# Kernel tuning notes

Hardware: AMD Instinct MI355X
Metric: run time of the kernel (lower is better)

The kernel has to match this reference:

```python
import jax, jax.numpy as jnp
import numpy as np

LOG2 = np.float32(np.log(2.0))

def _jsd_pos(p):
    # get_positive_expectation, measure='JSD', average=False
    return LOG2 - jax.nn.softplus(-p)

def setup_inputs() -> dict:
    key = jax.random.key(0)
    k1, k2, k3, k4, k5, k6 = jax.random.split(key, 6)
    N, G, D = 65536, 512, 256
    batch_1 = jnp.sort(jax.random.randint(k1, (N,), 0, G))
    batch_2 = jnp.sort(jax.random.randint(k2, (N,), 0, G))
    z1 = jax.random.normal(k3, (N, D), dtype=jnp.float32)
    z2 = jax.random.normal(k4, (N, D), dtype=jnp.float32)
    g1 = jax.random.normal(k5, (G, D), dtype=jnp.float32)
    g2 = jax.random.normal(k6, (G, D), dtype=jnp.float32)
    return {"batch_1": batch_1, "batch_2": batch_2, "z1": z1, "z2": z2, "g1": g1, "g2": g2}

def reference(batch_1, batch_2, z1, z2, g1, g2):
    # pos_mask scatter-build -> dense one-hot [N, G]
    pos_mask_1 = jax.nn.one_hot(batch_1, g1.shape[0], dtype=z1.dtype)
    pos_mask_2 = jax.nn.one_hot(batch_2, g2.shape[0], dtype=z2.dtype)
    # masked node-graph similarity matrices [N, G]
    self_sim_1 = (z1 @ g1.T) * pos_mask_1
    self_sim_2 = (z2 @ g2.T) * pos_mask_2
    cross_sim_12 = (z1 @ g2.T) * pos_mask_1
    cross_sim_21 = (z2 @ g1.T) * pos_mask_2
    # sep=True branch: per-node row sums, L2 distance over nodes
    self_js_11 = _jsd_pos(self_sim_1).sum(1)
    cross_js_12 = _jsd_pos(cross_sim_12).sum(1)
    self_js_22 = _jsd_pos(self_sim_2).sum(1)
    cross_js_21 = _jsd_pos(cross_sim_21).sum(1)
    L_1 = jnp.sqrt(jnp.sum((self_js_11 - cross_js_12) ** 2))
    L_2 = jnp.sqrt(jnp.sum((self_js_22 - cross_js_21) ** 2))
    return L_1 + L_2
```

## Files before the change

kernel.cpp:

```cpp
#include <hip/hip_runtime.h>
#include <math.h>

__device__ __forceinline__ float jsd_pos(float p) {
    float sp = fmaxf(-p, 0.0f) + log1pf(expf(-fabsf(p)));
    return 0.69314718055994531f - sp;
}

#define NBLOCKS 2048
#define NODES_PER_WAVE 8

__global__ __launch_bounds__(256) void jsd_dot_kernel(
    const int*   __restrict__ b1,
    const int*   __restrict__ b2,
    const float* __restrict__ z1,
    const float* __restrict__ z2,
    const float* __restrict__ g1,
    const float* __restrict__ g2,
    float*       __restrict__ partials)
{
    const int wave = threadIdx.x >> 6;
    const int lane = threadIdx.x & 63;
    const int w    = blockIdx.x * 4 + wave;

    float acc1 = 0.0f, acc2 = 0.0f;

    #pragma unroll
    for (int j = 0; j < NODES_PER_WAVE; ++j) {
        const int node = w * NODES_PER_WAVE + j;

        const int i1 = b1[node];
        const int i2 = b2[node];

        const float4 a1  = ((const float4*)(z1 + (size_t)node * 256))[lane];
        const float4 a2  = ((const float4*)(z2 + (size_t)node * 256))[lane];
        const float4 w11 = ((const float4*)(g1 + (size_t)i1 * 256))[lane];
        const float4 w12 = ((const float4*)(g2 + (size_t)i1 * 256))[lane];
        const float4 w22 = ((const float4*)(g2 + (size_t)i2 * 256))[lane];
        const float4 w21 = ((const float4*)(g1 + (size_t)i2 * 256))[lane];

        float s11 = a1.x*w11.x + a1.y*w11.y + a1.z*w11.z + a1.w*w11.w;
        float c12 = a1.x*w12.x + a1.y*w12.y + a1.z*w12.z + a1.w*w12.w;
        float s22 = a2.x*w22.x + a2.y*w22.y + a2.z*w22.z + a2.w*w22.w;
        float c21 = a2.x*w21.x + a2.y*w21.y + a2.z*w21.z + a2.w*w21.w;

        #pragma unroll
        for (int off = 32; off >= 1; off >>= 1) {
            s11 += __shfl_down(s11, off, 64);
            c12 += __shfl_down(c12, off, 64);
            s22 += __shfl_down(s22, off, 64);
            c21 += __shfl_down(c21, off, 64);
        }

        if (lane == 0) {
            float d1 = jsd_pos(s11) - jsd_pos(c12);
            float d2 = jsd_pos(s22) - jsd_pos(c21);
            acc1 += d1 * d1;
            acc2 += d2 * d2;
        }
    }

    __shared__ float s1[4], s2[4];
    if (lane == 0) { s1[wave] = acc1; s2[wave] = acc2; }
    __syncthreads();

    if (threadIdx.x == 0) {
        partials[blockIdx.x * 2 + 0] = s1[0] + s1[1] + s1[2] + s1[3];
        partials[blockIdx.x * 2 + 1] = s2[0] + s2[1] + s2[2] + s2[3];
    }
}

__global__ __launch_bounds__(256) void jsd_reduce_kernel(
    const float* __restrict__ partials,
    float*       __restrict__ out)
{
    const int tid  = threadIdx.x;
    const int wave = tid >> 6;
    const int lane = tid & 63;

    float a = 0.0f, b = 0.0f;
    for (int i = tid; i < NBLOCKS; i += 256) {
        a += partials[i * 2 + 0];
        b += partials[i * 2 + 1];
    }

    #pragma unroll
    for (int off = 32; off >= 1; off >>= 1) {
        a += __shfl_down(a, off, 64);
        b += __shfl_down(b, off, 64);
    }

    __shared__ float s1[4], s2[4];
    if (lane == 0) { s1[wave] = a; s2[wave] = b; }
    __syncthreads();

    if (tid == 0) {
        float t1 = s1[0] + s1[1] + s1[2] + s1[3];
        float t2 = s2[0] + s2[1] + s2[2] + s2[3];
        out[0] = sqrtf(t1) + sqrtf(t2);
    }
}

extern "C" void kernel_launch(void* const* d_in, const int* in_sizes, int n_in,
                              void* d_out, int out_size, void* d_ws, size_t ws_size,
                              hipStream_t stream) {
    const int*   b1 = (const int*)  d_in[0];
    const int*   b2 = (const int*)  d_in[1];
    const float* z1 = (const float*)d_in[2];
    const float* z2 = (const float*)d_in[3];
    const float* g1 = (const float*)d_in[4];
    const float* g2 = (const float*)d_in[5];
    float* out      = (float*)d_out;
    float* partials = (float*)d_ws;

    jsd_dot_kernel<<<NBLOCKS, 256, 0, stream>>>(b1, b2, z1, z2, g1, g2, partials);
    jsd_reduce_kernel<<<1, 256, 0, stream>>>(partials, out);
}
```

Before: 177.5 us.

## Use DPP wave reductions, batch loads up front, fast math, and smaller per-wave work

Replaces the shuffle-based wave reductions with DPP row-shift and row-broadcast sequences whose result lands in lane 63. All batch indices and z rows for a wave are loaded up front, with a scalarized base, so more memory requests are in flight before any gathers of the g rows. Softplus now uses fast __expf/__logf, and the JSD difference is rewritten algebraically. The grid doubles to 4096 blocks with 4 nodes per wave, and the reduce loop is fully unrolled. Fast intrinsics slightly reduce accuracy.

```diff
diff --git a/kernel.cpp b/kernel.cpp
--- a/kernel.cpp
+++ b/kernel.cpp
@@ -1,13 +1,33 @@
 #include <hip/hip_runtime.h>
 #include <math.h>
 
-__device__ __forceinline__ float jsd_pos(float p) {
-    float sp = fmaxf(-p, 0.0f) + log1pf(expf(-fabsf(p)));
-    return 0.69314718055994531f - sp;
+__device__ __forceinline__ float spn(float p) {
+    return fmaxf(-p, 0.0f) + __logf(1.0f + __expf(-fabsf(p)));
 }
 
-#define NBLOCKS 2048
-#define NODES_PER_WAVE 8
+__device__ __forceinline__ float dot4(float4 a, float4 b) {
+    return a.x * b.x + a.y * b.y + a.z * b.z + a.w * b.w;
+}
+
+__device__ __forceinline__ float wave64_reduce(float x) {
+    int t;
+    t = __builtin_amdgcn_update_dpp(0, __builtin_bit_cast(int, x), 0x111, 0xf, 0xf, true);
+    x += __builtin_bit_cast(float, t);
+    t = __builtin_amdgcn_update_dpp(0, __builtin_bit_cast(int, x), 0x112, 0xf, 0xf, true);
+    x += __builtin_bit_cast(float, t);
+    t = __builtin_amdgcn_update_dpp(0, __builtin_bit_cast(int, x), 0x114, 0xf, 0xf, true);
+    x += __builtin_bit_cast(float, t);
+    t = __builtin_amdgcn_update_dpp(0, __builtin_bit_cast(int, x), 0x118, 0xf, 0xf, true);
+    x += __builtin_bit_cast(float, t);
+    t = __builtin_amdgcn_update_dpp(0, __builtin_bit_cast(int, x), 0x142, 0xa, 0xf, true);
+    x += __builtin_bit_cast(float, t);
+    t = __builtin_amdgcn_update_dpp(0, __builtin_bit_cast(int, x), 0x143, 0xc, 0xf, true);
+    x += __builtin_bit_cast(float, t);
+    return x;
+}
+
+#define NBLOCKS 4096
+#define NODES_PER_WAVE 4
 
 __global__ __launch_bounds__(256) void jsd_dot_kernel(
     const int*   __restrict__ b1,
@@ -21,46 +41,48 @@
     const int wave = threadIdx.x >> 6;
     const int lane = threadIdx.x & 63;
     const int w    = blockIdx.x * 4 + wave;
+    const int base = w * NODES_PER_WAVE;
+
+    const int sbase = __builtin_amdgcn_readfirstlane(base);
+
+    int i1[NODES_PER_WAVE], i2[NODES_PER_WAVE];
+    #pragma unroll
+    for (int j = 0; j < NODES_PER_WAVE; ++j) {
+        i1[j] = b1[sbase + j];
+        i2[j] = b2[sbase + j];
+    }
+
+    float4 a1[NODES_PER_WAVE], a2[NODES_PER_WAVE];
+    #pragma unroll
+    for (int j = 0; j < NODES_PER_WAVE; ++j) {
+        a1[j] = ((const float4*)(z1 + (size_t)(sbase + j) * 256))[lane];
+        a2[j] = ((const float4*)(z2 + (size_t)(sbase + j) * 256))[lane];
+    }
 
     float acc1 = 0.0f, acc2 = 0.0f;
 
     #pragma unroll
     for (int j = 0; j < NODES_PER_WAVE; ++j) {
-        const int node = w * NODES_PER_WAVE + j;
+        const float4 w11 = ((const float4*)(g1 + (size_t)i1[j] * 256))[lane];
+        const float4 w12 = ((const float4*)(g2 + (size_t)i1[j] * 256))[lane];
+        const float4 w22 = ((const float4*)(g2 + (size_t)i2[j] * 256))[lane];
+        const float4 w21 = ((const float4*)(g1 + (size_t)i2[j] * 256))[lane];
 
-        const int i1 = b1[node];
-        const int i2 = b2[node];
+        float s11 = wave64_reduce(dot4(a1[j], w11));
+        float c12 = wave64_reduce(dot4(a1[j], w12));
+        float s22 = wave64_reduce(dot4(a2[j], w22));
+        float c21 = wave64_reduce(dot4(a2[j], w21));
 
-        const float4 a1  = ((const float4*)(z1 + (size_t)node * 256))[lane];
-        const float4 a2  = ((const float4*)(z2 + (size_t)node * 256))[lane];
-        const float4 w11 = ((const float4*)(g1 + (size_t)i1 * 256))[lane];
-        const float4 w12 = ((const float4*)(g2 + (size_t)i1 * 256))[lane];
-        const float4 w22 = ((const float4*)(g2 + (size_t)i2 * 256))[lane];
-        const float4 w21 = ((const float4*)(g1 + (size_t)i2 * 256))[lane];
-
-        float s11 = a1.x*w11.x + a1.y*w11.y + a1.z*w11.z + a1.w*w11.w;
-        float c12 = a1.x*w12.x + a1.y*w12.y + a1.z*w12.z + a1.w*w12.w;
-        float s22 = a2.x*w22.x + a2.y*w22.y + a2.z*w22.z + a2.w*w22.w;
-        float c21 = a2.x*w21.x + a2.y*w21.y + a2.z*w21.z + a2.w*w21.w;
-
-        #pragma unroll
-        for (int off = 32; off >= 1; off >>= 1) {
-            s11 += __shfl_down(s11, off, 64);
-            c12 += __shfl_down(c12, off, 64);
-            s22 += __shfl_down(s22, off, 64);
-            c21 += __shfl_down(c21, off, 64);
-        }
-
-        if (lane == 0) {
-            float d1 = jsd_pos(s11) - jsd_pos(c12);
-            float d2 = jsd_pos(s22) - jsd_pos(c21);
+        if (lane == 63) {
+            float d1 = spn(c12) - spn(s11);
+            float d2 = spn(c21) - spn(s22);
             acc1 += d1 * d1;
             acc2 += d2 * d2;
         }
     }
 
     __shared__ float s1[4], s2[4];
-    if (lane == 0) { s1[wave] = acc1; s2[wave] = acc2; }
+    if (lane == 63) { s1[wave] = acc1; s2[wave] = acc2; }
     __syncthreads();
 
     if (threadIdx.x == 0) {
@@ -78,19 +100,17 @@
     const int lane = tid & 63;
 
     float a = 0.0f, b = 0.0f;
-    for (int i = tid; i < NBLOCKS; i += 256) {
-        a += partials[i * 2 + 0];
-        b += partials[i * 2 + 1];
+    #pragma unroll
+    for (int i = 0; i < NBLOCKS / 256; ++i) {
+        a += partials[(i * 256 + tid) * 2 + 0];
+        b += partials[(i * 256 + tid) * 2 + 1];
     }
 
-    #pragma unroll
-    for (int off = 32; off >= 1; off >>= 1) {
-        a += __shfl_down(a, off, 64);
-        b += __shfl_down(b, off, 64);
-    }
+    a = wave64_reduce(a);
+    b = wave64_reduce(b);
 
     __shared__ float s1[4], s2[4];
-    if (lane == 0) { s1[wave] = a; s2[wave] = b; }
+    if (lane == 63) { s1[wave] = a; s2[wave] = b; }
     __syncthreads();
 
     if (tid == 0) {
```

After: 154.6 us. 12.9% less time.
